# Performance work log

Measured on AMD Instinct MI355X. Metric: run time of the kernel, lower is better.

Reference implementation:

```python
import jax, jax.numpy as jnp
import numpy as np
from jax import lax

B = 8          # batch
IMG = 224      # image size
PATCH = 16     # patch size / stride
D = 384        # embed_dim = d_model = d_inner (expand=1)
DEPTH = 24     # number of blocks
N = 16         # d_state
K = 4          # d_conv
R = 24         # dt_rank = ceil(D/16)
H = D * 4 * 2 // 3   # SwiGLU hidden = 1024
L = (IMG // PATCH) ** 2  # 196 tokens


def setup_inputs() -> dict:
    ks = iter(jax.random.split(jax.random.key(0), 40))
    def rn(shape, s=0.02):
        return jax.random.normal(next(ks), shape, jnp.float32) * s
    inp = {}
    inp["x"] = jax.random.normal(next(ks), (B, 3, IMG, IMG), jnp.float32)
    inp["patch_w"] = rn((D, 3, PATCH, PATCH))
    inp["patch_b"] = jnp.zeros((D,), jnp.float32)
    inp["norm1_w"] = jnp.ones((DEPTH, D), jnp.float32)
    inp["norm1_b"] = jnp.zeros((DEPTH, D), jnp.float32)
    inp["in_proj_w"] = rn((DEPTH, 2 * D, D))
    inp["conv_w"] = rn((DEPTH, D, K), 0.1)
    inp["conv_b"] = jnp.zeros((DEPTH, D), jnp.float32)
    inp["x_proj_w"] = rn((DEPTH, R + 2 * N, D))
    inp["dt_proj_w"] = rn((DEPTH, D, R), 0.1)
    inp["dt_proj_b"] = rn((DEPTH, D), 0.1)
    # S4D-real init: A = -exp(A_log), A_log = log(1..N)
    inp["A_log"] = jnp.tile(jnp.log(jnp.arange(1, N + 1, dtype=jnp.float32))[None, None, :], (DEPTH, D, 1))
    inp["D_skip"] = jnp.ones((DEPTH, D), jnp.float32)
    inp["out_proj_w"] = rn((DEPTH, D, D))
    inp["norm2_w"] = jnp.ones((DEPTH, D), jnp.float32)
    inp["norm2_b"] = jnp.zeros((DEPTH, D), jnp.float32)
    inp["w1_w"] = rn((DEPTH, H, D)); inp["w1_b"] = jnp.zeros((DEPTH, H), jnp.float32)
    inp["w2_w"] = rn((DEPTH, H, D)); inp["w2_b"] = jnp.zeros((DEPTH, H), jnp.float32)
    inp["w3_w"] = rn((DEPTH, D, H)); inp["w3_b"] = jnp.zeros((DEPTH, D), jnp.float32)
    inp["normf_w"] = jnp.ones((D,), jnp.float32)
    inp["normf_b"] = jnp.zeros((D,), jnp.float32)
    return inp


def _ln(x, w, b, eps=1e-5):
    m = x.mean(-1, keepdims=True)
    v = jnp.mean((x - m) ** 2, axis=-1, keepdims=True)
    return (x - m) / jnp.sqrt(v + eps) * w + b


def _mamba(x, in_w, cw, cb, xp_w, dtw, dtb, a_log, d_skip, ow):
    # x: [B, L, D]; Mamba with expand=1, bimamba 'none'
    bsz, seq, _ = x.shape
    xz = jnp.einsum('bld,ed->ble', x, in_w)        # [B, L, 2D]
    xc, z = jnp.split(xz, 2, axis=-1)
    # causal depthwise conv1d, kernel K, padding K-1, truncated to L
    xpd = jnp.pad(xc, ((0, 0), (K - 1, 0), (0, 0)))
    xconv = sum(xpd[:, k:k + seq, :] * cw[:, k] for k in range(K)) + cb
    xa = jax.nn.silu(xconv)
    dbc = jnp.einsum('bld,ed->ble', xa, xp_w)      # [B, L, R+2N]
    dt = jax.nn.softplus(jnp.einsum('blr,dr->bld', dbc[..., :R], dtw) + dtb)  # [B, L, D]
    Bm = dbc[..., R:R + N]                         # [B, L, N]
    Cm = dbc[..., R + N:]                          # [B, L, N]
    A = -jnp.exp(a_log)                            # [D, N]

    def step(h, t):
        dt_t, B_t, C_t, x_t = t                    # [B,D],[B,N],[B,N],[B,D]
        h = h * jnp.exp(dt_t[..., None] * A) + (dt_t * x_t)[..., None] * B_t[:, None, :]
        return h, jnp.einsum('bdn,bn->bd', h, C_t)

    h0 = jnp.zeros((bsz, D, N), x.dtype)
    _, ys = lax.scan(step, h0, (dt.transpose(1, 0, 2), Bm.transpose(1, 0, 2),
                                Cm.transpose(1, 0, 2), xa.transpose(1, 0, 2)))
    y = ys.transpose(1, 0, 2) + d_skip * xa
    y = y * jax.nn.silu(z)
    return jnp.einsum('bld,ed->ble', y, ow)


def _forward(x, patch_w, patch_b, norm1_w, norm1_b, in_proj_w, conv_w, conv_b,
             x_proj_w, dt_proj_w, dt_proj_b, A_log, D_skip, out_proj_w,
             norm2_w, norm2_b, w1_w, w1_b, w2_w, w2_b, w3_w, w3_b, normf_w, normf_b):
    p = lax.conv_general_dilated(x, patch_w, (PATCH, PATCH), 'VALID',
                                 dimension_numbers=('NCHW', 'OIHW', 'NCHW'))
    p = p + patch_b[None, :, None, None]
    h = p.reshape(p.shape[0], D, -1).transpose(0, 2, 1)   # [B, L, D]
    for i in range(DEPTH):
        h = h + _mamba(_ln(h, norm1_w[i], norm1_b[i]), in_proj_w[i], conv_w[i], conv_b[i],
                       x_proj_w[i], dt_proj_w[i], dt_proj_b[i], A_log[i], D_skip[i], out_proj_w[i])
        hn = _ln(h, norm2_w[i], norm2_b[i])
        hid = jax.nn.silu(hn @ w1_w[i].T + w1_b[i]) * (hn @ w2_w[i].T + w2_b[i])
        h = h + hid @ w3_w[i].T + w3_b[i]
    return _ln(h, normf_w, normf_b)


def reference(x, patch_w, patch_b, norm1_w, norm1_b, in_proj_w, conv_w, conv_b,
              x_proj_w, dt_proj_w, dt_proj_b, A_log, D_skip, out_proj_w,
              norm2_w, norm2_b, w1_w, w1_b, w2_w, w2_b, w3_w, w3_b, normf_w, normf_b):
    return _forward(x, patch_w, patch_b, norm1_w, norm1_b, in_proj_w, conv_w, conv_b,
                    x_proj_w, dt_proj_w, dt_proj_b, A_log, D_skip, out_proj_w,
                    norm2_w, norm2_b, w1_w, w1_b, w2_w, w2_b, w3_w, w3_b, normf_w, normf_b)
```

## Files before the change

kernel.cpp:

```cpp
#include <hip/hip_runtime.h>
#include <math.h>

#define BB 8
#define LL 196
#define DD 384
#define NDEPTH 24
#define NST 16
#define RRANK 24
#define HHID 1024
#define MROWS (BB*LL)
#define NCH 28
#define CHL 7

typedef float f32x4 __attribute__((ext_vector_type(4)));
typedef short s16x8 __attribute__((ext_vector_type(8)));
typedef short s16x4 __attribute__((ext_vector_type(4)));
typedef __bf16 b16x8 __attribute__((ext_vector_type(8)));
typedef unsigned short u16;
typedef unsigned int u32;

#if defined(__has_builtin)
#  if __has_builtin(__builtin_amdgcn_global_load_lds)
#    define HAS_GLL 1
#  endif
#endif
#ifndef HAS_GLL
#  define HAS_GLL 0
#endif

__device__ __forceinline__ float sigmoidf_(float x){ return 1.f/(1.f+__expf(-x)); }

__device__ __forceinline__ u16 f2bf(float f){
    u32 u = __builtin_bit_cast(u32, f);
    u32 r = (u + 0x7fffu + ((u >> 16) & 1u)) >> 16;
    return (u16)r;
}
__device__ __forceinline__ float bf2f(u16 v){
    u32 u = ((u32)v) << 16;
    return __builtin_bit_cast(float, u);
}

__device__ __forceinline__ void gll16(const u16* g, void* lds){
#if HAS_GLL
    __builtin_amdgcn_global_load_lds(
        (const __attribute__((address_space(1))) unsigned int*)g,
        (__attribute__((address_space(3))) unsigned int*)lds, 16, 0, 0);
#endif
}

template<int N> __device__ __forceinline__ void waitbar(){
    if constexpr (N==0) asm volatile("s_waitcnt vmcnt(0) lgkmcnt(0)\ns_barrier" ::: "memory");
    else if constexpr (N==4) asm volatile("s_waitcnt vmcnt(4) lgkmcnt(0)\ns_barrier" ::: "memory");
    else if constexpr (N==8) asm volatile("s_waitcnt vmcnt(8) lgkmcnt(0)\ns_barrier" ::: "memory");
    else asm volatile("s_waitcnt vmcnt(0) lgkmcnt(0)\ns_barrier" ::: "memory");
    __builtin_amdgcn_sched_barrier(0);
}
__device__ __forceinline__ void bar_release(){
    asm volatile("s_waitcnt lgkmcnt(0)\ns_barrier" ::: "memory");
    __builtin_amdgcn_sched_barrier(0);
}

template<typename V>
__device__ __forceinline__ auto mfma_try(V a, V b, f32x4 c, int)
    -> decltype(__builtin_amdgcn_mfma_f32_16x16x32_bf16(a, b, c, 0, 0, 0))
{ return __builtin_amdgcn_mfma_f32_16x16x32_bf16(a, b, c, 0, 0, 0); }

template<typename V>
__device__ __forceinline__ f32x4 mfma_try(V a, V b, f32x4 c, long)
{
    return __builtin_amdgcn_mfma_f32_16x16x32_bf16(
        __builtin_bit_cast(b16x8, a), __builtin_bit_cast(b16x8, b), c, 0, 0, 0);
}
__device__ __forceinline__ f32x4 mfma_bf16(s16x8 a, s16x8 b, f32x4 c){ return mfma_try(a, b, c, 0); }

__global__ __launch_bounds__(64) void ln_k(const float* __restrict__ X,
    const float* __restrict__ w, const float* __restrict__ b, float* __restrict__ Y)
{
    int row = blockIdx.x;
    int lane = threadIdx.x;
    const float* x = X + (size_t)row*DD;
    float v[6]; float s=0.f, s2=0.f;
    #pragma unroll
    for (int j=0;j<6;j++){ float t = x[lane + j*64]; v[j]=t; s+=t; s2+=t*t; }
    #pragma unroll
    for (int o=32;o>=1;o>>=1){ s += __shfl_xor(s,o); s2 += __shfl_xor(s2,o); }
    float m = s*(1.f/DD);
    float var = s2*(1.f/DD) - m*m;
    float rstd = rsqrtf(var + 1e-5f);
    #pragma unroll
    for (int j=0;j<6;j++){
        int c = lane + j*64;
        Y[(size_t)row*DD + c] = (v[j]-m)*rstd*w[c] + b[c];
    }
}

__global__ void gather_k(const float* __restrict__ x, u16* __restrict__ P)
{
    int idx = blockIdx.x*blockDim.x + threadIdx.x;
    if (idx >= MROWS*768) return;
    int k = idx % 768;
    int bl = idx / 768;
    int l = bl % LL;
    int b = bl / LL;
    int c = k >> 8;
    int rem = k & 255;
    int dy = rem >> 4, dx = rem & 15;
    int py = l / 14, px = l % 14;
    P[idx] = f2bf(x[(((size_t)b*3 + c)*224 + (py*16+dy))*224 + (px*16+dx)]);
}

__device__ __forceinline__ int swz(int row, int chunk){
    return (row << 7) + ((chunk ^ (row & 7)) << 4);
}

template<int EPI, bool WB, int CFG, int PRO, int K>
__global__ __launch_bounds__(256) void mgemm_k(
    const u16* __restrict__ A, const float* __restrict__ Af,
    const float* __restrict__ lnw, const float* __restrict__ lnb,
    const void* __restrict__ W1v, const void* __restrict__ W2v,
    const float* __restrict__ bias1, const float* __restrict__ bias2,
    float* __restrict__ Cf, u16* __restrict__ Cb,
    int M, int N)
{
    constexpr int  BM   = (CFG==1)?32:16;
    constexpr int  FM   = (CFG==2)?1:2;
    constexpr int  FN   = 2;
    constexpr int  NAR  = (BM+31)/32;
    constexpr bool DUAL = (EPI==4);
    constexpr bool RES  = (EPI==2 || EPI==3);
    constexpr int  ABY  = BM*128;
    constexpr int  BBY  = 128*128;
    constexpr bool ASY  = WB && (HAS_GLL==1);
    constexpr int  NKT  = K >> 6;
    constexpr int  NLW  = DUAL ? 8 : 4;
    __shared__ __attribute__((aligned(16))) char sm[2*ABY + 2*BBY + (DUAL ? 2*BBY : 0)];
    char* A0 = sm;          char* A1 = sm + ABY;
    char* B0 = sm + 2*ABY;  char* B1 = B0 + BBY;
    char* C0 = B1 + BBY;    char* C1 = C0 + BBY;

    const int tid = threadIdx.x;
    const int row0 = blockIdx.y * BM;
    const int col0 = blockIdx.x << 7;
    const int w = tid >> 6, lane = tid & 63;
    const int wn  = w;
    const int lr = lane & 15, lk = lane >> 4;
    const int ar0 = tid >> 3, ac8 = tid & 7;
    const bool apart = (CFG != 2) || (tid < 128);

    const u16*   W1b = (const u16*)W1v;
    const u16*   W2b = (const u16*)W2v;
    const float* W1f = (const float*)W1v;
    const float* W2f = (const float*)W2v;

    f32x4 acc [FM][FN] = {};
    f32x4 acc2[FM][FN] = {};

    float cres[FM][FN][4];
    if (RES){
        #pragma unroll
        for (int n=0;n<FN;n++){
            int gc = col0 + wn*32 + n*16 + lr;
            #pragma unroll
            for (int m=0;m<FM;m++){
                #pragma unroll
                for (int r=0;r<4;r++){
                    int gr = row0 + m*16 + lk*4 + r;
                    cres[m][n][r] = (gc < N && gr < M) ? Cf[(size_t)gr*N + gc] : 0.f;
                }
            }
        }
    }

    s16x8 aval[NAR];
    s16x8 bval[4], b2val[4];
    float4 bvf[8], b2vf[8];
    s16x8 lnr[(PRO==1)?NKT:1];

    if (PRO == 1 && apart){
        const float* xrow = Af + (size_t)(row0 + ar0)*DD;
        float4 va[6], vb[6];
        float s = 0.f, s2 = 0.f;
        #pragma unroll
        for (int j=0;j<6;j++){
            va[j] = *(const float4*)(xrow + j*64 + ac8*8);
            vb[j] = *(const float4*)(xrow + j*64 + ac8*8 + 4);
            s  += va[j].x+va[j].y+va[j].z+va[j].w + vb[j].x+vb[j].y+vb[j].z+vb[j].w;
            s2 += va[j].x*va[j].x+va[j].y*va[j].y+va[j].z*va[j].z+va[j].w*va[j].w
                + vb[j].x*vb[j].x+vb[j].y*vb[j].y+vb[j].z*vb[j].z+vb[j].w*vb[j].w;
        }
        #pragma unroll
        for (int o=1;o<8;o<<=1){ s += __shfl_xor(s,o); s2 += __shfl_xor(s2,o); }
        float m = s*(1.f/DD);
        float rstd = rsqrtf(s2*(1.f/DD) - m*m + 1e-5f);
        #pragma unroll
        for (int j=0;j<6;j++){
            int c0 = j*64 + ac8*8;
            float4 w0 = *(const float4*)(lnw + c0);
            float4 w1 = *(const float4*)(lnw + c0 + 4);
            float4 b0 = *(const float4*)(lnb + c0);
            float4 b1 = *(const float4*)(lnb + c0 + 4);
            s16x8 ov;
            ov[0]=(short)f2bf((va[j].x-m)*rstd*w0.x+b0.x);
            ov[1]=(short)f2bf((va[j].y-m)*rstd*w0.y+b0.y);
            ov[2]=(short)f2bf((va[j].z-m)*rstd*w0.z+b0.z);
            ov[3]=(short)f2bf((va[j].w-m)*rstd*w0.w+b0.w);
            ov[4]=(short)f2bf((vb[j].x-m)*rstd*w1.x+b1.x);
            ov[5]=(short)f2bf((vb[j].y-m)*rstd*w1.y+b1.y);
            ov[6]=(short)f2bf((vb[j].z-m)*rstd*w1.z+b1.z);
            ov[7]=(short)f2bf((vb[j].w-m)*rstd*w1.w+b1.w);
            if (j < NKT) lnr[j] = ov;
        }
    }

    auto stageAsync = [&](int kt, char* bA, char* bB, char* bC){
        const int lhi = lane >> 3, llo = lane & 7;
        const int colel = (kt << 6) + ((llo ^ lhi) << 3);
        if (PRO == 0){
            constexpr int ACH = BM/8;
            #pragma unroll
            for (int ci = w; ci < ACH; ci += 4){
                int gr = row0 + ci*8 + lhi;
                gll16(A + (size_t)gr*K + colel, bA + ci*1024);
            }
        }
        #pragma unroll
        for (int i=0;i<4;i++){
            int ci = w*4 + i;
            int gb = col0 + ci*8 + lhi;
            gll16(W1b + (size_t)gb*K + colel, bB + ci*1024);
        }
        if (DUAL){
            #pragma unroll
            for (int i=0;i<4;i++){
                int ci = w*4 + i;
                int gb = col0 + ci*8 + lhi;
                gll16(W2b + (size_t)gb*K + colel, bC + ci*1024);
            }
        }
    };

    auto loadT = [&](int kt){
        const int kb = kt << 6;
        if (PRO == 0 && apart){
            #pragma unroll
            for (int i=0;i<NAR;i++){
                int gr = row0 + i*32 + ar0;
                if (gr < M) aval[i] = *(const s16x8*)(A + (size_t)gr*K + kb + ac8*8);
                else        aval[i] = s16x8{0,0,0,0,0,0,0,0};
            }
        }
        if (WB){
            #pragma unroll
            for (int i=0;i<4;i++){
                int gb = col0 + i*32 + ar0;
                if (gb < N) bval[i] = *(const s16x8*)(W1b + (size_t)gb*K + kb + ac8*8);
                else        bval[i] = s16x8{0,0,0,0,0,0,0,0};
            }
            if (DUAL){
                #pragma unroll
                for (int i=0;i<4;i++){
                    int gb = col0 + i*32 + ar0;
                    if (gb < N) b2val[i] = *(const s16x8*)(W2b + (size_t)gb*K + kb + ac8*8);
                    else        b2val[i] = s16x8{0,0,0,0,0,0,0,0};
                }
            }
        } else {
            #pragma unroll
            for (int i=0;i<8;i++){
                int ss = i*256 + tid;
                int r = ss >> 4, q = ss & 15;
                int gb = col0 + r;
                if (gb < N) bvf[i] = *(const float4*)(W1f + (size_t)gb*K + kb + q*4);
                else        bvf[i] = float4{0,0,0,0};
            }
            if (DUAL){
                #pragma unroll
                for (int i=0;i<8;i++){
                    int ss = i*256 + tid;
                    int r = ss >> 4, q = ss & 15;
                    int gb = col0 + r;
                    if (gb < N) b2vf[i] = *(const float4*)(W2f + (size_t)gb*K + kb + q*4);
                    else        b2vf[i] = float4{0,0,0,0};
                }
            }
        }
    };
    auto writeT = [&](char* bA, char* bB, char* bC){
        if (PRO == 0 && apart){
            #pragma unroll
            for (int i=0;i<NAR;i++)
                *(s16x8*)(bA + swz(i*32 + ar0, ac8)) = aval[i];
        }
        if (WB){
            #pragma unroll
            for (int i=0;i<4;i++)
                *(s16x8*)(bB + swz(i*32 + ar0, ac8)) = bval[i];
            if (DUAL){
                #pragma unroll
                for (int i=0;i<4;i++)
                    *(s16x8*)(bC + swz(i*32 + ar0, ac8)) = b2val[i];
            }
        } else {
            #pragma unroll
            for (int i=0;i<8;i++){
                int ss = i*256 + tid;
                int r = ss >> 4, q = ss & 15;
                float4 v = bvf[i];
                s16x4 cv = { (short)f2bf(v.x), (short)f2bf(v.y), (short)f2bf(v.z), (short)f2bf(v.w) };
                int off = (r << 7) + (((q >> 1) ^ (r & 7)) << 4) + ((q & 1) << 3);
                *(s16x4*)(bB + off) = cv;
            }
            if (DUAL){
                #pragma unroll
                for (int i=0;i<8;i++){
                    int ss = i*256 + tid;
                    int r = ss >> 4, q = ss & 15;
                    float4 v = b2vf[i];
                    s16x4 cv = { (short)f2bf(v.x), (short)f2bf(v.y), (short)f2bf(v.z), (short)f2bf(v.w) };
                    int off = (r << 7) + (((q >> 1) ^ (r & 7)) << 4) + ((q & 1) << 3);
                    *(s16x4*)(bC + off) = cv;
                }
            }
        }
    };

    auto compute = [&](char* cA, char* cB, char* cC){
        #pragma unroll
        for (int ks=0; ks<2; ks++){
            s16x8 af[FM], bfr[FN];
            #pragma unroll
            for (int m=0;m<FM;m++)
                af[m] = *(const s16x8*)(cA + swz(m*16 + lr, ks*4 + lk));
            #pragma unroll
            for (int n=0;n<FN;n++)
                bfr[n] = *(const s16x8*)(cB + swz(wn*32 + n*16 + lr, ks*4 + lk));
            #pragma unroll
            for (int m=0;m<FM;m++)
                #pragma unroll
                for (int n=0;n<FN;n++)
                    acc[m][n] = mfma_bf16(af[m], bfr[n], acc[m][n]);
            if (DUAL){
                s16x8 b2r[FN];
                #pragma unroll
                for (int n=0;n<FN;n++)
                    b2r[n] = *(const s16x8*)(cC + swz(wn*32 + n*16 + lr, ks*4 + lk));
                #pragma unroll
                for (int m=0;m<FM;m++)
                    #pragma unroll
                    for (int n=0;n<FN;n++)
                        acc2[m][n] = mfma_bf16(af[m], b2r[n], acc2[m][n]);
            }
        }
    };

    if (ASY){
        stageAsync(0, A0, B0, C0);
        if (NKT > 1) stageAsync(1, A1, B1, C1);
        if (PRO == 1 && apart){
            *(s16x8*)(A0 + swz(ar0, ac8)) = lnr[0];
            if (NKT > 1) *(s16x8*)(A1 + swz(ar0, ac8)) = lnr[(1 < NKT) ? 1 : 0];
        }
        if (NKT > 1) waitbar<NLW>(); else waitbar<0>();
        #pragma unroll
        for (int kt=0; kt<NKT; kt++){
            if (kt & 1) compute(A1, B1, C1);
            else        compute(A0, B0, C0);
            if (kt+1 < NKT){
                bar_release();
                if (kt+2 < NKT){
                    char* rA = (kt&1)?A1:A0; char* rB = (kt&1)?B1:B0; char* rC = (kt&1)?C1:C0;
                    stageAsync(kt+2, rA, rB, rC);
                    if (PRO == 1 && apart)
                        *(s16x8*)(rA + swz(ar0, ac8)) = lnr[(kt+2 < NKT) ? (kt+2) : 0];
                    waitbar<NLW>();
                } else {
                    waitbar<0>();
                }
            }
        }
    } else {
        loadT(0); writeT(A0, B0, C0);
        if (PRO == 1 && apart) *(s16x8*)(A0 + swz(ar0, ac8)) = lnr[0];
        __syncthreads();
        #pragma unroll
        for (int kt=0; kt<NKT; kt++){
            const bool more = (kt+1 < NKT);
            char* nA = (kt&1)?A0:A1; char* nB = (kt&1)?B0:B1; char* nC = (kt&1)?C0:C1;
            if (more){
                loadT(kt+1);
                if (PRO == 1 && apart) *(s16x8*)(nA + swz(ar0, ac8)) = lnr[(kt+1 < NKT) ? (kt+1) : 0];
            }
            if (kt & 1) compute(A1, B1, C1);
            else        compute(A0, B0, C0);
            if (more) writeT(nA, nB, nC);
            __syncthreads();
        }
    }

    #pragma unroll
    for (int n=0;n<FN;n++){
        int gc = col0 + wn*32 + n*16 + lr;
        if (gc >= N) continue;
        float b1 = 0.f, b2 = 0.f;
        if (EPI==1||EPI==3||EPI==4) b1 = bias1[gc];
        if (EPI==4) b2 = bias2[gc];
        #pragma unroll
        for (int m=0;m<FM;m++){
            #pragma unroll
            for (int r=0;r<4;r++){
                int gr = row0 + m*16 + lk*4 + r;
                if (gr >= M) continue;
                float v = acc[m][n][r];
                if (EPI==1||EPI==3) v += b1;
                if (RES) v += cres[m][n][r];
                if (EPI==4){
                    float v1 = v + b1;
                    float v2 = acc2[m][n][r] + b2;
                    Cb[(size_t)gr*N + gc] = f2bf(v1 * sigmoidf_(v1) * v2);
                } else if (EPI==6){
                    Cb[(size_t)gr*N + gc] = f2bf(v);
                } else {
                    Cf[(size_t)gr*N + gc] = v;
                }
            }
        }
    }
}

__global__ void cvtw_k(const float* __restrict__ s, u16* __restrict__ d, int n)
{
    int i = blockIdx.x*blockDim.x + threadIdx.x;
    int idx = i*4;
    if (idx + 4 <= n){
        float4 v = *(const float4*)(s + idx);
        s16x4 cv = { (short)f2bf(v.x), (short)f2bf(v.y), (short)f2bf(v.z), (short)f2bf(v.w) };
        *(s16x4*)(d + idx) = cv;
    } else {
        for (int j=idx;j<n;j++) d[j] = f2bf(s[j]);
    }
}

__global__ __launch_bounds__(384) void scanA_k(
    const float* __restrict__ Wx, const u16* __restrict__ xzb,
    const float* __restrict__ cw, const float* __restrict__ cb,
    const float* __restrict__ dtw, const float* __restrict__ dtb,
    const float* __restrict__ a_log,
    float* __restrict__ Pout, float* __restrict__ Sout,
    float2* __restrict__ dtxv, float* __restrict__ dbc)
{
    __shared__ float xaS[CHL][DD+4];
    __shared__ float Ds[CHL][56];
    int b = blockIdx.x / NCH;
    int c = blockIdx.x % NCH;
    int d = threadIdx.x;

    float cwr[4];
    #pragma unroll
    for (int k=0;k<4;k++) cwr[k] = cw[d*4+k];
    float cbv = cb[d];
    int l0 = c*CHL;
    float p3=0.f, p2=0.f, p1=0.f;
    if (l0 >= 3) p3 = bf2f(xzb[(size_t)(b*LL+l0-3)*768 + d]);
    if (l0 >= 2) p2 = bf2f(xzb[(size_t)(b*LL+l0-2)*768 + d]);
    if (l0 >= 1) p1 = bf2f(xzb[(size_t)(b*LL+l0-1)*768 + d]);
    float xv[CHL];
    #pragma unroll
    for (int j=0;j<CHL;j++){
        int row = b*LL + l0 + j;
        float cur = bf2f(xzb[(size_t)row*768 + d]);
        float a = cbv;
        a = fmaf(p3, cwr[0], a); a = fmaf(p2, cwr[1], a);
        a = fmaf(p1, cwr[2], a); a = fmaf(cur, cwr[3], a);
        p3 = p2; p2 = p1; p1 = cur;
        xv[j] = a * sigmoidf_(a);
        xaS[j][d] = xv[j];
    }
    __syncthreads();

    for (int t = d; t < CHL*56; t += 384){
        int q = t / CHL, j = t - q*CHL;
        const float* Wr = Wx + (size_t)q*DD;
        float accd = 0.f;
        #pragma unroll 8
        for (int dd=0; dd<DD; dd+=4){
            float4 wv = *(const float4*)(Wr + dd);
            accd = fmaf(xaS[j][dd],   wv.x, accd);
            accd = fmaf(xaS[j][dd+1], wv.y, accd);
            accd = fmaf(xaS[j][dd+2], wv.z, accd);
            accd = fmaf(xaS[j][dd+3], wv.w, accd);
        }
        Ds[j][q] = accd;
        dbc[(size_t)(b*LL + l0 + j)*56 + q] = accd;
    }
    __syncthreads();

    float dtwr[RRANK];
    #pragma unroll
    for (int r=0;r<RRANK;r++) dtwr[r] = dtw[d*RRANK + r];
    float dtbv = dtb[d];
    float Aa[NST];
    #pragma unroll
    for (int n=0;n<NST;n++) Aa[n] = -__expf(a_log[d*NST+n]);
    float hst[NST], P[NST];
    #pragma unroll
    for (int n=0;n<NST;n++){ hst[n]=0.f; P[n]=1.f; }
    #pragma unroll
    for (int j=0;j<CHL;j++){
        int row = b*LL + l0 + j;
        float t = dtbv;
        #pragma unroll
        for (int r=0;r<RRANK;r++) t = fmaf(dtwr[r], Ds[j][r], t);
        float dtv = (t > 20.f) ? t : log1pf(__expf(t));
        dtxv[(size_t)row*DD + d] = float2{dtv, xv[j]};
        float du = dtv*xv[j];
        #pragma unroll
        for (int n=0;n<NST;n++){
            float e = __expf(dtv*Aa[n]);
            hst[n] = fmaf(hst[n], e, du*Ds[j][24+n]);
            P[n] *= e;
        }
    }
    size_t base = ((size_t)(b*NCH + c)*DD + d)*NST;
    #pragma unroll
    for (int n=0;n<NST;n++){ Pout[base+n]=P[n]; Sout[base+n]=hst[n]; }
}

__global__ __launch_bounds__(384) void scanC_k(
    const float* __restrict__ dbc, const float2* __restrict__ dtxv,
    const u16* __restrict__ xzb, const float* __restrict__ a_log,
    const float* __restrict__ Pin, const float* __restrict__ Sin,
    const float* __restrict__ dskip,
    u16* __restrict__ yg)
{
    int b = blockIdx.x / NCH;
    int c = blockIdx.x % NCH;
    int d = threadIdx.x;
    __shared__ float Ds[CHL][56];
    for (int t = threadIdx.x; t < CHL*56; t += 384){
        int j = t/56, q = t%56;
        Ds[j][q] = dbc[(size_t)(b*LL + c*CHL + j)*56 + q];
    }
    __syncthreads();
    float hst[NST];
    #pragma unroll
    for (int n=0;n<NST;n++) hst[n]=0.f;
    for (int cc=0; cc<c; cc++){
        size_t base = ((size_t)(b*NCH + cc)*DD + d)*NST;
        #pragma unroll
        for (int n=0;n<NST;n++)
            hst[n] = fmaf(Pin[base+n], hst[n], Sin[base+n]);
    }
    float Aa[NST];
    #pragma unroll
    for (int n=0;n<NST;n++) Aa[n] = -__expf(a_log[d*NST+n]);
    float dsk = dskip[d];
    int l0 = c*CHL;
    #pragma unroll
    for (int j=0;j<CHL;j++){
        int row = b*LL + l0 + j;
        float2 dx = dtxv[(size_t)row*DD + d];
        float dtv = dx.x, xv = dx.y;
        float du = dtv*xv;
        float y = 0.f;
        #pragma unroll
        for (int n=0;n<NST;n++){
            float e = __expf(dtv*Aa[n]);
            hst[n] = fmaf(hst[n], e, du*Ds[j][24+n]);
            y = fmaf(hst[n], Ds[j][40+n], y);
        }
        float zv = bf2f(xzb[(size_t)row*768 + 384 + d]);
        float g = zv * sigmoidf_(zv);
        yg[(size_t)row*DD + d] = f2bf((y + dsk*xv)*g);
    }
}

template<int EPI, int CFG, int PRO, int K>
static void mg(bool wb, dim3 g, hipStream_t s,
               const void* A, const float* Af, const float* lnw, const float* lnb,
               const void* Wb, const void* Wf, const void* W2b, const void* W2f,
               const float* b1, const float* b2, float* Cf, u16* Cb,
               int M, int N)
{
    if (wb) mgemm_k<EPI,true ,CFG,PRO,K><<<g,256,0,s>>>((const u16*)A, Af, lnw, lnb, Wb, W2b, b1, b2, Cf, Cb, M, N);
    else    mgemm_k<EPI,false,CFG,PRO,K><<<g,256,0,s>>>((const u16*)A, Af, lnw, lnb, Wf, W2f, b1, b2, Cf, Cb, M, N);
}

extern "C" void kernel_launch(void* const* d_in, const int* in_sizes, int n_in,
                              void* d_out, int out_size, void* d_ws, size_t ws_size,
                              hipStream_t stream)
{
    const float* x         = (const float*)d_in[0];
    const float* patch_w   = (const float*)d_in[1];
    const float* patch_b   = (const float*)d_in[2];
    const float* norm1_w   = (const float*)d_in[3];
    const float* norm1_b   = (const float*)d_in[4];
    const float* in_proj_w = (const float*)d_in[5];
    const float* conv_w    = (const float*)d_in[6];
    const float* conv_b    = (const float*)d_in[7];
    const float* x_proj_w  = (const float*)d_in[8];
    const float* dt_w      = (const float*)d_in[9];
    const float* dt_b      = (const float*)d_in[10];
    const float* A_log     = (const float*)d_in[11];
    const float* D_skip    = (const float*)d_in[12];
    const float* out_w     = (const float*)d_in[13];
    const float* norm2_w   = (const float*)d_in[14];
    const float* norm2_b   = (const float*)d_in[15];
    const float* w1_w      = (const float*)d_in[16];
    const float* w1_b      = (const float*)d_in[17];
    const float* w2_w      = (const float*)d_in[18];
    const float* w2_b      = (const float*)d_in[19];
    const float* w3_w      = (const float*)d_in[20];
    const float* w3_b      = (const float*)d_in[21];
    const float* normf_w   = (const float*)d_in[22];
    const float* normf_b   = (const float*)d_in[23];

    char* wsb = (char*)d_ws;
    size_t o = 0;
    auto take = [&](size_t bytes) -> char* {
        char* p = wsb + o;
        o += (bytes + 255) & ~(size_t)255;
        return p;
    };

    float* h    = (float*)take((size_t)602112*4);
    float* dbc  = (float*)take((size_t)87808*4);
    float* Pb   = (float*)take((size_t)BB*NCH*DD*NST*4);
    float* Sb   = (float*)take((size_t)BB*NCH*DD*NST*4);
    float2* dtxv= (float2*)take((size_t)MROWS*DD*8);
    u16*  xzb   = (u16*)take((size_t)1204224*2);
    u16*  yg    = (u16*)take((size_t)602112*2);
    u16*  hid   = (u16*)take((size_t)1605632*2);
    u16*  patches = hid;

    const size_t NPW = 294912, NIN = 7077888, NOUT = 3538944,
                 NW1 = 9437184, NW2 = 9437184, NW3 = 9437184;
    u16* wcP = (u16*)take(NPW*2);
    u16* wcI = (u16*)take(NIN*2);
    u16* wcO = (u16*)take(NOUT*2);
    u16* wc1 = (u16*)take(NW1*2);
    u16* wc2 = (u16*)take(NW2*2);
    u16* wc3 = (u16*)take(NW3*2);
    bool wb = (ws_size >= o);

    if (wb){
        cvtw_k<<<(int)((NPW/4+255)/256), 256, 0, stream>>>(patch_w, wcP, (int)NPW);
        cvtw_k<<<(int)((NIN/4+255)/256), 256, 0, stream>>>(in_proj_w, wcI, (int)NIN);
        cvtw_k<<<(int)((NOUT/4+255)/256),256, 0, stream>>>(out_w, wcO, (int)NOUT);
        cvtw_k<<<(int)((NW1/4+255)/256), 256, 0, stream>>>(w1_w, wc1, (int)NW1);
        cvtw_k<<<(int)((NW2/4+255)/256), 256, 0, stream>>>(w2_w, wc2, (int)NW2);
        cvtw_k<<<(int)((NW3/4+255)/256), 256, 0, stream>>>(w3_w, wc3, (int)NW3);
    }

    const int GY32 = MROWS/32;
    const int GY16 = MROWS/16;

    gather_k<<<(MROWS*768+255)/256, 256, 0, stream>>>(x, patches);
    mg<1,2,0,768>(wb, dim3(3,GY16), stream, patches, nullptr, nullptr, nullptr,
              wcP, patch_w, nullptr, nullptr, patch_b, nullptr, h, nullptr, MROWS, DD);

    for (int i=0;i<NDEPTH;i++){
        mg<6,1,1,384>(wb, dim3(6,GY32), stream, nullptr, h, norm1_w + i*DD, norm1_b + i*DD,
                  wcI + (size_t)i*768*DD, in_proj_w + (size_t)i*768*DD, nullptr, nullptr,
                  nullptr, nullptr, nullptr, xzb, MROWS, 768);
        scanA_k<<<BB*NCH, 384, 0, stream>>>(x_proj_w + (size_t)i*56*DD, xzb,
                                            conv_w + i*DD*4, conv_b + i*DD,
                                            dt_w + (size_t)i*DD*RRANK, dt_b + i*DD,
                                            A_log + (size_t)i*DD*NST, Pb, Sb, dtxv, dbc);
        scanC_k<<<BB*NCH, 384, 0, stream>>>(dbc, dtxv, xzb, A_log + (size_t)i*DD*NST,
                                            Pb, Sb, D_skip + i*DD, yg);
        mg<2,2,0,384>(wb, dim3(3,GY16), stream, yg, nullptr, nullptr, nullptr,
                  wcO + (size_t)i*DD*DD, out_w + (size_t)i*DD*DD, nullptr, nullptr,
                  nullptr, nullptr, h, nullptr, MROWS, DD);
        mg<4,1,1,384>(wb, dim3(8,GY32), stream, nullptr, h, norm2_w + i*DD, norm2_b + i*DD,
                  wc1 + (size_t)i*HHID*DD, w1_w + (size_t)i*HHID*DD,
                  wc2 + (size_t)i*HHID*DD, w2_w + (size_t)i*HHID*DD,
                  w1_b + i*HHID, w2_b + i*HHID, nullptr, hid, MROWS, HHID);
        mg<3,2,0,1024>(wb, dim3(3,GY16), stream, hid, nullptr, nullptr, nullptr,
                  wc3 + (size_t)i*DD*HHID, w3_w + (size_t)i*DD*HHID, nullptr, nullptr,
                  w3_b + i*DD, nullptr, h, nullptr, MROWS, DD);
    }

    ln_k<<<MROWS, 64, 0, stream>>>(h, normf_w, normf_b, (float*)d_out);
}
```

Baseline: 2.216 ms.

## Fuse out_proj GEMM into scan kernel epilogue with FP32 dot products

The scanC kernel now keeps the gated scan output for its 7-token chunk in shared memory and computes the out_proj matmul itself, adding the result to the residual h directly. This removes the bf16 yg buffer round trip, one GEMM launch per layer, and the out_proj weight conversion. In exchange the projection runs on scalar FP32 FMAs instead of matrix cores: each thread streams a full 384-float weight row from global memory, and the 224 blocks each reread the whole weight matrix, so the arithmetic and weight traffic may cost more than the removed GEMM.

```diff
diff --git a/kernel.cpp b/kernel.cpp
--- a/kernel.cpp
+++ b/kernel.cpp
@@ -529,13 +529,14 @@
     const float* __restrict__ dbc, const float2* __restrict__ dtxv,
     const u16* __restrict__ xzb, const float* __restrict__ a_log,
     const float* __restrict__ Pin, const float* __restrict__ Sin,
-    const float* __restrict__ dskip,
-    u16* __restrict__ yg)
-{
+    const float* __restrict__ dskip, const float* __restrict__ Wo,
+    float* __restrict__ h)
+{
+    __shared__ float ygS[CHL][DD+4];
+    __shared__ float Ds[CHL][56];
     int b = blockIdx.x / NCH;
     int c = blockIdx.x % NCH;
     int d = threadIdx.x;
-    __shared__ float Ds[CHL][56];
     for (int t = threadIdx.x; t < CHL*56; t += 384){
         int j = t/56, q = t%56;
         Ds[j][q] = dbc[(size_t)(b*LL + c*CHL + j)*56 + q];
@@ -570,7 +571,29 @@
         }
         float zv = bf2f(xzb[(size_t)row*768 + 384 + d]);
         float g = zv * sigmoidf_(zv);
-        yg[(size_t)row*DD + d] = f2bf((y + dsk*xv)*g);
+        ygS[j][d] = (y + dsk*xv)*g;
+    }
+    __syncthreads();
+
+    const float* Wr = Wo + (size_t)d*DD;
+    float o[CHL];
+    #pragma unroll
+    for (int j=0;j<CHL;j++) o[j] = 0.f;
+    #pragma unroll 4
+    for (int dd=0; dd<DD; dd+=4){
+        float4 wv = *(const float4*)(Wr + dd);
+        #pragma unroll
+        for (int j=0;j<CHL;j++){
+            o[j] = fmaf(ygS[j][dd],   wv.x, o[j]);
+            o[j] = fmaf(ygS[j][dd+1], wv.y, o[j]);
+            o[j] = fmaf(ygS[j][dd+2], wv.z, o[j]);
+            o[j] = fmaf(ygS[j][dd+3], wv.w, o[j]);
+        }
+    }
+    #pragma unroll
+    for (int j=0;j<CHL;j++){
+        size_t idx = (size_t)(b*LL + l0 + j)*DD + d;
+        h[idx] += o[j];
     }
 }
 
@@ -628,15 +651,13 @@
     float* Sb   = (float*)take((size_t)BB*NCH*DD*NST*4);
     float2* dtxv= (float2*)take((size_t)MROWS*DD*8);
     u16*  xzb   = (u16*)take((size_t)1204224*2);
-    u16*  yg    = (u16*)take((size_t)602112*2);
     u16*  hid   = (u16*)take((size_t)1605632*2);
     u16*  patches = hid;
 
-    const size_t NPW = 294912, NIN = 7077888, NOUT = 3538944,
+    const size_t NPW = 294912, NIN = 7077888,
                  NW1 = 9437184, NW2 = 9437184, NW3 = 9437184;
     u16* wcP = (u16*)take(NPW*2);
     u16* wcI = (u16*)take(NIN*2);
-    u16* wcO = (u16*)take(NOUT*2);
     u16* wc1 = (u16*)take(NW1*2);
     u16* wc2 = (u16*)take(NW2*2);
     u16* wc3 = (u16*)take(NW3*2);
@@ -645,7 +666,6 @@
     if (wb){
         cvtw_k<<<(int)((NPW/4+255)/256), 256, 0, stream>>>(patch_w, wcP, (int)NPW);
         cvtw_k<<<(int)((NIN/4+255)/256), 256, 0, stream>>>(in_proj_w, wcI, (int)NIN);
-        cvtw_k<<<(int)((NOUT/4+255)/256),256, 0, stream>>>(out_w, wcO, (int)NOUT);
         cvtw_k<<<(int)((NW1/4+255)/256), 256, 0, stream>>>(w1_w, wc1, (int)NW1);
         cvtw_k<<<(int)((NW2/4+255)/256), 256, 0, stream>>>(w2_w, wc2, (int)NW2);
         cvtw_k<<<(int)((NW3/4+255)/256), 256, 0, stream>>>(w3_w, wc3, (int)NW3);
@@ -667,10 +687,8 @@
                                             dt_w + (size_t)i*DD*RRANK, dt_b + i*DD,
                                             A_log + (size_t)i*DD*NST, Pb, Sb, dtxv, dbc);
         scanC_k<<<BB*NCH, 384, 0, stream>>>(dbc, dtxv, xzb, A_log + (size_t)i*DD*NST,
-                                            Pb, Sb, D_skip + i*DD, yg);
-        mg<2,2,0,384>(wb, dim3(3,GY16), stream, yg, nullptr, nullptr, nullptr,
-                  wcO + (size_t)i*DD*DD, out_w + (size_t)i*DD*DD, nullptr, nullptr,
-                  nullptr, nullptr, h, nullptr, MROWS, DD);
+                                            Pb, Sb, D_skip + i*DD,
+                                            out_w + (size_t)i*DD*DD, h);
         mg<4,1,1,384>(wb, dim3(8,GY32), stream, nullptr, h, norm2_w + i*DD, norm2_b + i*DD,
                   wc1 + (size_t)i*HHID*DD, w1_w + (size_t)i*HHID*DD,
                   wc2 + (size_t)i*HHID*DD, w2_w + (size_t)i*HHID*DD,
```

Measured after the change: 2.589 ms. 16.8% more time.
